# Performance work log

Hardware: AMD Instinct MI355X
Metric: run time of the kernel (lower is better)

The kernel has to match this reference:

```python
import jax, jax.numpy as jnp
import numpy as np

T, N = 512, 256          # timesteps, parallel envs
STATE, HID = 64, 128     # input features, GRU hidden size


def setup_inputs() -> dict:
    key = jax.random.key(0)
    k = jax.random.split(key, 6)
    inputs = jax.random.normal(k[0], (T * N, STATE), dtype=jnp.float32)
    hxs = jax.random.normal(k[1], (N, HID), dtype=jnp.float32)
    masks = (jax.random.uniform(k[2], (T * N, 1)) > 0.02).astype(jnp.float32)
    # GRU params (torch layout: gates ordered r, z, n; rows = 3*HID)
    weight_ih = jax.random.normal(k[3], (3 * HID, STATE), dtype=jnp.float32) * 0.1
    weight_hh = jax.random.normal(k[4], (3 * HID, HID), dtype=jnp.float32) * 0.1
    bias_ih = jnp.zeros((3 * HID,), dtype=jnp.float32)  # init.constant_(0)
    bias_hh = jnp.zeros((3 * HID,), dtype=jnp.float32)
    return {
        "inputs": inputs, "hxs": hxs, "masks": masks,
        "weight_ih": weight_ih, "weight_hh": weight_hh,
        "bias_ih": bias_ih, "bias_hh": bias_hh,
    }


def reference(inputs, hxs, masks, weight_ih, weight_hh, bias_ih, bias_hh):
    n, hid = hxs.shape
    t = inputs.shape[0] // n
    x = inputs.reshape(t, n, -1)       # (t, n, state)
    m = masks.reshape(t, n, 1)         # (t, n, 1)

    # Input-to-gate projections are mask-independent: precompute for all steps.
    gx = jnp.einsum('tns,gs->tng', x, weight_ih) + bias_ih  # (t, n, 3H)

    def step(h, xs):
        gx_t, m_t = xs
        h = h * m_t                                 # inline reset (fused; replaces chunk splitting)
        gh = h @ weight_hh.T + bias_hh              # (n, 3H)
        xr, xz, xn = jnp.split(gx_t, 3, axis=-1)
        hr, hz, hn = jnp.split(gh, 3, axis=-1)
        r = jax.nn.sigmoid(xr + hr)
        z = jax.nn.sigmoid(xz + hz)
        cand = jnp.tanh(xn + r * hn)
        h = (1.0 - z) * cand + z * h                # torch GRU update
        return h, h

    h_final, ys = jax.lax.scan(step, hxs, (gx, m))  # ys: (t, n, H)
    return ys.reshape(t * n, hid), h_final
```

## Files before the change

### kernel.cpp

```cpp
#include <hip/hip_runtime.h>
#include <math.h>

#define T_STEPS  512
#define N_ENVS   256
#define STATE    64
#define HID      128
#define NTHREADS 512

typedef _Float16 half8   __attribute__((ext_vector_type(8)));
typedef _Float16 half2_t __attribute__((ext_vector_type(2)));
typedef float    floatx4 __attribute__((ext_vector_type(4)));

__device__ __forceinline__ float sigmoid_fast(float v) {
    return __builtin_amdgcn_rcpf(1.f + __expf(-v));
}
__device__ __forceinline__ float tanh_fast(float v) {
    const float e  = __expf(-2.f * fabsf(v));
    const float mg = (1.f - e) * __builtin_amdgcn_rcpf(1.f + e);
    return copysignf(mg, v);
}

__global__ __launch_bounds__(NTHREADS, 2) void gru_mfma8(
    const float* __restrict__ x,
    const float* __restrict__ h0,
    const float* __restrict__ masks,
    const float* __restrict__ wih,
    const float* __restrict__ whh,
    const float* __restrict__ bih,
    const float* __restrict__ bhh,
    float* __restrict__ out)
{
    const int b    = blockIdx.x;
    const int tid  = threadIdx.x;
    const int w    = tid >> 6;
    const int lane = tid & 63;
    const int c    = lane & 15;
    const int quad = lane >> 4;
    const int j    = 16 * w + c;

    __shared__ __align__(16) _Float16 buf[2][192];
    __shared__ __align__(16) float    xstage[2][16][STATE];
    __shared__ __align__(16) float    ring[2][16][HID];
    __shared__ float ms[32];

    const int rowb[3] = { j, HID + j, 2 * HID + j };
    half8 B[3][6];
#pragma unroll
    for (int ti = 0; ti < 3; ++ti) {
        const int g = rowb[ti];
#pragma unroll
        for (int kt = 0; kt < 6; ++kt) {
            const float* src = (kt < 4) ? (whh + (size_t)g * HID + kt * 32 + quad * 8)
                                        : (wih + (size_t)g * STATE + (kt - 4) * 32 + quad * 8);
            const float4 p0 = *(const float4*)(src);
            const float4 p1 = *(const float4*)(src + 4);
            half8 hb;
            hb[0] = (_Float16)p0.x; hb[1] = (_Float16)p0.y;
            hb[2] = (_Float16)p0.z; hb[3] = (_Float16)p0.w;
            hb[4] = (_Float16)p1.x; hb[5] = (_Float16)p1.y;
            hb[6] = (_Float16)p1.z; hb[7] = (_Float16)p1.w;
            B[ti][kt] = hb;
        }
    }

    const float br  = bih[j] + bhh[j];
    const float bz  = bih[HID + j] + bhh[HID + j];
    const float bhn = bhh[2 * HID + j];
    const float bxn = bih[2 * HID + j];

    float hr = h0[(size_t)b * HID + j];
    const float m0 = masks[b];
    float hm = m0 * hr;
    if (quad == 0) buf[0][j] = (_Float16)hm;
    if (tid < 32) {
        const float2 xv = *(const float2*)(x + (size_t)b * STATE + 2 * tid);
        half2_t hx = { (_Float16)xv.x, (_Float16)xv.y };
        *(half2_t*)&buf[0][128 + 2 * tid] = hx;
    }
    float4 xp = {0.f, 0.f, 0.f, 0.f};
    if (tid < 256) {
        const int k = tid >> 4, cc = (tid & 15) * 4;
        *(float4*)&xstage[0][k][cc] =
            *(const float4*)(x + ((size_t)(1 + k) * N_ENVS + b) * STATE + cc);
        xp = *(const float4*)(x + ((size_t)(17 + k) * N_ENVS + b) * STATE + cc);
    }
    float mreg = 0.f;
    if (tid < 16) {
        ms[tid] = masks[(size_t)tid * N_ENVS + b];
        mreg = masks[(size_t)(16 + tid) * N_ENVS + b];
    }
    __syncthreads();

    const floatx4 zero4 = {0.f, 0.f, 0.f, 0.f};

    for (int tc = 0; tc < 32; ++tc) {
        if (tc > 0) {
            const int k = tid >> 5, jj = (tid & 31) * 4;
            *(float4*)(out + ((size_t)((tc - 1) * 16 + k) * N_ENVS + b) * HID + jj) =
                *(const float4*)&ring[(tc - 1) & 1][k][jj];
        }
        if (tid < 256) {
            const int k = tid >> 4, cc = (tid & 15) * 4;
            *(float4*)&xstage[(tc + 1) & 1][k][cc] = xp;
            const int st = (tc + 2) * 16 + 1 + k;
            if (st < T_STEPS)
                xp = *(const float4*)(x + ((size_t)st * N_ENVS + b) * STATE + cc);
        }
        if (tid < 16) {
            ms[(tc * 16 + 16 + tid) & 31] = mreg;
            const int st = tc * 16 + 32 + tid;
            if (st < T_STEPS) mreg = masks[(size_t)st * N_ENVS + b];
        }

#pragma unroll
        for (int s = 0; s < 16; ++s) {
            const int t = tc * 16 + s;
            const _Float16* bufc = buf[s & 1];
            _Float16* bufn = (_Float16*)buf[(s + 1) & 1];

            half8 a0 = *(const half8*)(bufc + 0 * 32 + quad * 8);
            half8 a1 = *(const half8*)(bufc + 1 * 32 + quad * 8);
            half8 a2 = *(const half8*)(bufc + 2 * 32 + quad * 8);
            half8 a3 = *(const half8*)(bufc + 3 * 32 + quad * 8);
            half8 a4 = *(const half8*)(bufc + 4 * 32 + quad * 8);
            half8 a5 = *(const half8*)(bufc + 5 * 32 + quad * 8);

            floatx4 r_a = __builtin_amdgcn_mfma_f32_16x16x32_f16(a0, B[0][0], zero4, 0, 0, 0);
            floatx4 r_b = __builtin_amdgcn_mfma_f32_16x16x32_f16(a3, B[0][3], zero4, 0, 0, 0);
            floatx4 z_a = __builtin_amdgcn_mfma_f32_16x16x32_f16(a0, B[1][0], zero4, 0, 0, 0);
            floatx4 z_b = __builtin_amdgcn_mfma_f32_16x16x32_f16(a3, B[1][3], zero4, 0, 0, 0);
            floatx4 hn4 = __builtin_amdgcn_mfma_f32_16x16x32_f16(a0, B[2][0], zero4, 0, 0, 0);
            floatx4 xn4 = __builtin_amdgcn_mfma_f32_16x16x32_f16(a4, B[2][4], zero4, 0, 0, 0);
            r_a = __builtin_amdgcn_mfma_f32_16x16x32_f16(a1, B[0][1], r_a, 0, 0, 0);
            r_b = __builtin_amdgcn_mfma_f32_16x16x32_f16(a4, B[0][4], r_b, 0, 0, 0);
            z_a = __builtin_amdgcn_mfma_f32_16x16x32_f16(a1, B[1][1], z_a, 0, 0, 0);
            z_b = __builtin_amdgcn_mfma_f32_16x16x32_f16(a4, B[1][4], z_b, 0, 0, 0);
            hn4 = __builtin_amdgcn_mfma_f32_16x16x32_f16(a1, B[2][1], hn4, 0, 0, 0);
            xn4 = __builtin_amdgcn_mfma_f32_16x16x32_f16(a5, B[2][5], xn4, 0, 0, 0);
            r_a = __builtin_amdgcn_mfma_f32_16x16x32_f16(a2, B[0][2], r_a, 0, 0, 0);
            r_b = __builtin_amdgcn_mfma_f32_16x16x32_f16(a5, B[0][5], r_b, 0, 0, 0);
            z_a = __builtin_amdgcn_mfma_f32_16x16x32_f16(a2, B[1][2], z_a, 0, 0, 0);
            z_b = __builtin_amdgcn_mfma_f32_16x16x32_f16(a5, B[1][5], z_b, 0, 0, 0);
            hn4 = __builtin_amdgcn_mfma_f32_16x16x32_f16(a2, B[2][2], hn4, 0, 0, 0);
            hn4 = __builtin_amdgcn_mfma_f32_16x16x32_f16(a3, B[2][3], hn4, 0, 0, 0);

            const float ur = (r_a[0] + r_b[0]) + br;
            const float uz = (z_a[0] + z_b[0]) + bz;
            const float hn = hn4[0] + bhn;
            const float xn = xn4[0] + bxn;
            const float r  = sigmoid_fast(ur);
            const float z  = sigmoid_fast(uz);
            const float cd = tanh_fast(fmaf(r, hn, xn));
            const float hnew = fmaf(z, hm - cd, cd);

            if (quad == 0) ring[tc & 1][s][j] = hnew;
            if (t < T_STEPS - 1) {
                const float mn = ms[(t + 1) & 31];
                hm = mn * hnew;
                if (quad == 0) bufn[j] = (_Float16)hm;
                if (w == (s & 7) && lane < 32) {
                    const float2 xv = *(const float2*)&xstage[tc & 1][s][2 * lane];
                    half2_t hx = { (_Float16)xv.x, (_Float16)xv.y };
                    *(half2_t*)&bufn[128 + 2 * lane] = hx;
                }
            }
            hr = hnew;
            __syncthreads();
        }
    }

    {
        const int k = tid >> 5, jj = (tid & 31) * 4;
        *(float4*)(out + ((size_t)(496 + k) * N_ENVS + b) * HID + jj) =
            *(const float4*)&ring[1][k][jj];
    }
    if (quad == 0)
        out[(size_t)T_STEPS * N_ENVS * HID + (size_t)b * HID + j] = hr;
}

extern "C" void kernel_launch(void* const* d_in, const int* in_sizes, int n_in,
                              void* d_out, int out_size, void* d_ws, size_t ws_size,
                              hipStream_t stream) {
    const float* x   = (const float*)d_in[0];
    const float* h0  = (const float*)d_in[1];
    const float* mk  = (const float*)d_in[2];
    const float* wih = (const float*)d_in[3];
    const float* whh = (const float*)d_in[4];
    const float* bih = (const float*)d_in[5];
    const float* bhh = (const float*)d_in[6];
    float* out = (float*)d_out;

    hipLaunchKernelGGL(gru_mfma8, dim3(N_ENVS), dim3(NTHREADS), 0, stream,
                       x, h0, mk, wih, whh, bih, bhh, out);
}
```

Baseline: 338.0 us.

## Hoist input projection out of recurrent step into per-chunk batched MFMA

Rather than folding x_t into each step's A operand (6 K-tiles per step), the kernel now computes the input-to-gate projection for 16 timesteps at once per chunk. It does this with batched MFMAs (16 timesteps as the M dimension), stores the results in shared memory, and reads them per step. The serial recurrent step drops from 18 to 12 MFMAs and no longer stages x into the A buffer. The cost is extra shared memory (gxp is 32KB, which may affect the 2-blocks-per-CU occupancy), an extra barrier per chunk, and per-step LDS float4 reads.

Result: faster. 305.1 us (-9.7%).

```diff
diff --git a/kernel.cpp b/kernel.cpp
--- a/kernel.cpp
+++ b/kernel.cpp
@@ -8,7 +8,7 @@
 #define NTHREADS 512
 
 typedef _Float16 half8   __attribute__((ext_vector_type(8)));
-typedef _Float16 half2_t __attribute__((ext_vector_type(2)));
+typedef _Float16 half4_t __attribute__((ext_vector_type(4)));
 typedef float    floatx4 __attribute__((ext_vector_type(4)));
 
 __device__ __forceinline__ float sigmoid_fast(float v) {
@@ -20,7 +20,7 @@
     return copysignf(mg, v);
 }
 
-__global__ __launch_bounds__(NTHREADS, 2) void gru_mfma8(
+__global__ __launch_bounds__(NTHREADS, 2) void gru_mfma_split(
     const float* __restrict__ x,
     const float* __restrict__ h0,
     const float* __restrict__ masks,
@@ -38,20 +38,20 @@
     const int quad = lane >> 4;
     const int j    = 16 * w + c;
 
-    __shared__ __align__(16) _Float16 buf[2][192];
-    __shared__ __align__(16) float    xstage[2][16][STATE];
+    __shared__ __align__(16) _Float16 buf[2][HID];
+    __shared__ __align__(16) _Float16 xh[2][16][STATE];
+    __shared__ __align__(16) float    gxp[16][HID][4];
     __shared__ __align__(16) float    ring[2][16][HID];
     __shared__ float ms[32];
 
     const int rowb[3] = { j, HID + j, 2 * HID + j };
-    half8 B[3][6];
+    half8 Bh[3][4];
 #pragma unroll
     for (int ti = 0; ti < 3; ++ti) {
         const int g = rowb[ti];
 #pragma unroll
-        for (int kt = 0; kt < 6; ++kt) {
-            const float* src = (kt < 4) ? (whh + (size_t)g * HID + kt * 32 + quad * 8)
-                                        : (wih + (size_t)g * STATE + (kt - 4) * 32 + quad * 8);
+        for (int kt = 0; kt < 4; ++kt) {
+            const float* src = whh + (size_t)g * HID + kt * 32 + quad * 8;
             const float4 p0 = *(const float4*)(src);
             const float4 p1 = *(const float4*)(src + 4);
             half8 hb;
@@ -59,7 +59,24 @@
             hb[2] = (_Float16)p0.z; hb[3] = (_Float16)p0.w;
             hb[4] = (_Float16)p1.x; hb[5] = (_Float16)p1.y;
             hb[6] = (_Float16)p1.z; hb[7] = (_Float16)p1.w;
-            B[ti][kt] = hb;
+            Bh[ti][kt] = hb;
+        }
+    }
+    half8 Bx[3][2];
+#pragma unroll
+    for (int ti = 0; ti < 3; ++ti) {
+        const int g = rowb[ti];
+#pragma unroll
+        for (int kt = 0; kt < 2; ++kt) {
+            const float* src = wih + (size_t)g * STATE + kt * 32 + quad * 8;
+            const float4 p0 = *(const float4*)(src);
+            const float4 p1 = *(const float4*)(src + 4);
+            half8 hb;
+            hb[0] = (_Float16)p0.x; hb[1] = (_Float16)p0.y;
+            hb[2] = (_Float16)p0.z; hb[3] = (_Float16)p0.w;
+            hb[4] = (_Float16)p1.x; hb[5] = (_Float16)p1.y;
+            hb[6] = (_Float16)p1.z; hb[7] = (_Float16)p1.w;
+            Bx[ti][kt] = hb;
         }
     }
 
@@ -72,17 +89,14 @@
     const float m0 = masks[b];
     float hm = m0 * hr;
     if (quad == 0) buf[0][j] = (_Float16)hm;
-    if (tid < 32) {
-        const float2 xv = *(const float2*)(x + (size_t)b * STATE + 2 * tid);
-        half2_t hx = { (_Float16)xv.x, (_Float16)xv.y };
-        *(half2_t*)&buf[0][128 + 2 * tid] = hx;
-    }
+
     float4 xp = {0.f, 0.f, 0.f, 0.f};
     if (tid < 256) {
         const int k = tid >> 4, cc = (tid & 15) * 4;
-        *(float4*)&xstage[0][k][cc] =
-            *(const float4*)(x + ((size_t)(1 + k) * N_ENVS + b) * STATE + cc);
-        xp = *(const float4*)(x + ((size_t)(17 + k) * N_ENVS + b) * STATE + cc);
+        const float4 xv = *(const float4*)(x + ((size_t)k * N_ENVS + b) * STATE + cc);
+        half4_t hx = {(_Float16)xv.x, (_Float16)xv.y, (_Float16)xv.z, (_Float16)xv.w};
+        *(half4_t*)&xh[0][k][cc] = hx;
+        xp = *(const float4*)(x + ((size_t)(16 + k) * N_ENVS + b) * STATE + cc);
     }
     float mreg = 0.f;
     if (tid < 16) {
@@ -101,8 +115,9 @@
         }
         if (tid < 256) {
             const int k = tid >> 4, cc = (tid & 15) * 4;
-            *(float4*)&xstage[(tc + 1) & 1][k][cc] = xp;
-            const int st = (tc + 2) * 16 + 1 + k;
+            half4_t hx = {(_Float16)xp.x, (_Float16)xp.y, (_Float16)xp.z, (_Float16)xp.w};
+            *(half4_t*)&xh[(tc + 1) & 1][k][cc] = hx;
+            const int st = (tc + 2) * 16 + k;
             if (st < T_STEPS)
                 xp = *(const float4*)(x + ((size_t)st * N_ENVS + b) * STATE + cc);
         }
@@ -112,6 +127,26 @@
             if (st < T_STEPS) mreg = masks[(size_t)st * N_ENVS + b];
         }
 
+        {
+            const _Float16* xr = &xh[tc & 1][c][0];
+            half8 ax0 = *(const half8*)&xr[quad * 8];
+            half8 ax1 = *(const half8*)&xr[32 + quad * 8];
+            floatx4 g0 = __builtin_amdgcn_mfma_f32_16x16x32_f16(ax0, Bx[0][0], zero4, 0, 0, 0);
+            floatx4 g1 = __builtin_amdgcn_mfma_f32_16x16x32_f16(ax0, Bx[1][0], zero4, 0, 0, 0);
+            floatx4 g2 = __builtin_amdgcn_mfma_f32_16x16x32_f16(ax0, Bx[2][0], zero4, 0, 0, 0);
+            g0 = __builtin_amdgcn_mfma_f32_16x16x32_f16(ax1, Bx[0][1], g0, 0, 0, 0);
+            g1 = __builtin_amdgcn_mfma_f32_16x16x32_f16(ax1, Bx[1][1], g1, 0, 0, 0);
+            g2 = __builtin_amdgcn_mfma_f32_16x16x32_f16(ax1, Bx[2][1], g2, 0, 0, 0);
+#pragma unroll
+            for (int i = 0; i < 4; ++i) {
+                const int s4 = quad * 4 + i;
+                gxp[s4][j][0] = g0[i];
+                gxp[s4][j][1] = g1[i];
+                gxp[s4][j][2] = g2[i];
+            }
+        }
+        __syncthreads();
+
 #pragma unroll
         for (int s = 0; s < 16; ++s) {
             const int t = tc * 16 + s;
@@ -122,32 +157,26 @@
             half8 a1 = *(const half8*)(bufc + 1 * 32 + quad * 8);
             half8 a2 = *(const half8*)(bufc + 2 * 32 + quad * 8);
             half8 a3 = *(const half8*)(bufc + 3 * 32 + quad * 8);
-            half8 a4 = *(const half8*)(bufc + 4 * 32 + quad * 8);
-            half8 a5 = *(const half8*)(bufc + 5 * 32 + quad * 8);
-
-            floatx4 r_a = __builtin_amdgcn_mfma_f32_16x16x32_f16(a0, B[0][0], zero4, 0, 0, 0);
-            floatx4 r_b = __builtin_amdgcn_mfma_f32_16x16x32_f16(a3, B[0][3], zero4, 0, 0, 0);
-            floatx4 z_a = __builtin_amdgcn_mfma_f32_16x16x32_f16(a0, B[1][0], zero4, 0, 0, 0);
-            floatx4 z_b = __builtin_amdgcn_mfma_f32_16x16x32_f16(a3, B[1][3], zero4, 0, 0, 0);
-            floatx4 hn4 = __builtin_amdgcn_mfma_f32_16x16x32_f16(a0, B[2][0], zero4, 0, 0, 0);
-            floatx4 xn4 = __builtin_amdgcn_mfma_f32_16x16x32_f16(a4, B[2][4], zero4, 0, 0, 0);
-            r_a = __builtin_amdgcn_mfma_f32_16x16x32_f16(a1, B[0][1], r_a, 0, 0, 0);
-            r_b = __builtin_amdgcn_mfma_f32_16x16x32_f16(a4, B[0][4], r_b, 0, 0, 0);
-            z_a = __builtin_amdgcn_mfma_f32_16x16x32_f16(a1, B[1][1], z_a, 0, 0, 0);
-            z_b = __builtin_amdgcn_mfma_f32_16x16x32_f16(a4, B[1][4], z_b, 0, 0, 0);
-            hn4 = __builtin_amdgcn_mfma_f32_16x16x32_f16(a1, B[2][1], hn4, 0, 0, 0);
-            xn4 = __builtin_amdgcn_mfma_f32_16x16x32_f16(a5, B[2][5], xn4, 0, 0, 0);
-            r_a = __builtin_amdgcn_mfma_f32_16x16x32_f16(a2, B[0][2], r_a, 0, 0, 0);
-            r_b = __builtin_amdgcn_mfma_f32_16x16x32_f16(a5, B[0][5], r_b, 0, 0, 0);
-            z_a = __builtin_amdgcn_mfma_f32_16x16x32_f16(a2, B[1][2], z_a, 0, 0, 0);
-            z_b = __builtin_amdgcn_mfma_f32_16x16x32_f16(a5, B[1][5], z_b, 0, 0, 0);
-            hn4 = __builtin_amdgcn_mfma_f32_16x16x32_f16(a2, B[2][2], hn4, 0, 0, 0);
-            hn4 = __builtin_amdgcn_mfma_f32_16x16x32_f16(a3, B[2][3], hn4, 0, 0, 0);
-
-            const float ur = (r_a[0] + r_b[0]) + br;
-            const float uz = (z_a[0] + z_b[0]) + bz;
-            const float hn = hn4[0] + bhn;
-            const float xn = xn4[0] + bxn;
+
+            floatx4 r_a = __builtin_amdgcn_mfma_f32_16x16x32_f16(a0, Bh[0][0], zero4, 0, 0, 0);
+            floatx4 r_b = __builtin_amdgcn_mfma_f32_16x16x32_f16(a2, Bh[0][2], zero4, 0, 0, 0);
+            floatx4 z_a = __builtin_amdgcn_mfma_f32_16x16x32_f16(a0, Bh[1][0], zero4, 0, 0, 0);
+            floatx4 z_b = __builtin_amdgcn_mfma_f32_16x16x32_f16(a2, Bh[1][2], zero4, 0, 0, 0);
+            floatx4 n_a = __builtin_amdgcn_mfma_f32_16x16x32_f16(a0, Bh[2][0], zero4, 0, 0, 0);
+            floatx4 n_b = __builtin_amdgcn_mfma_f32_16x16x32_f16(a2, Bh[2][2], zero4, 0, 0, 0);
+            r_a = __builtin_amdgcn_mfma_f32_16x16x32_f16(a1, Bh[0][1], r_a, 0, 0, 0);
+            r_b = __builtin_amdgcn_mfma_f32_16x16x32_f16(a3, Bh[0][3], r_b, 0, 0, 0);
+            z_a = __builtin_amdgcn_mfma_f32_16x16x32_f16(a1, Bh[1][1], z_a, 0, 0, 0);
+            z_b = __builtin_amdgcn_mfma_f32_16x16x32_f16(a3, Bh[1][3], z_b, 0, 0, 0);
+            n_a = __builtin_amdgcn_mfma_f32_16x16x32_f16(a1, Bh[2][1], n_a, 0, 0, 0);
+            n_b = __builtin_amdgcn_mfma_f32_16x16x32_f16(a3, Bh[2][3], n_b, 0, 0, 0);
+
+            const float4 gx4 = *(const float4*)&gxp[s][j][0];
+
+            const float ur = (r_a[0] + r_b[0]) + gx4.x + br;
+            const float uz = (z_a[0] + z_b[0]) + gx4.y + bz;
+            const float hn = (n_a[0] + n_b[0]) + bhn;
+            const float xn = gx4.z + bxn;
             const float r  = sigmoid_fast(ur);
             const float z  = sigmoid_fast(uz);
             const float cd = tanh_fast(fmaf(r, hn, xn));
@@ -158,11 +187,6 @@
                 const float mn = ms[(t + 1) & 31];
                 hm = mn * hnew;
                 if (quad == 0) bufn[j] = (_Float16)hm;
-                if (w == (s & 7) && lane < 32) {
-                    const float2 xv = *(const float2*)&xstage[tc & 1][s][2 * lane];
-                    half2_t hx = { (_Float16)xv.x, (_Float16)xv.y };
-                    *(half2_t*)&bufn[128 + 2 * lane] = hx;
-                }
             }
             hr = hnew;
             __syncthreads();
@@ -190,6 +214,6 @@
     const float* bhh = (const float*)d_in[6];
     float* out = (float*)d_out;
 
-    hipLaunchKernelGGL(gru_mfma8, dim3(N_ENVS), dim3(NTHREADS), 0, stream,
+    hipLaunchKernelGGL(gru_mfma_split, dim3(N_ENVS), dim3(NTHREADS), 0, stream,
                        x, h0, mk, wih, whh, bih, bhh, out);
 }
```
